# Kernel tuning notes

Hardware: AMD Instinct MI355X
Metric: run time of the kernel (lower is better)

## Reference

```python
import jax, jax.numpy as jnp
import numpy as np

CH = 256            # channels
IN_C = CH // 2      # 128
INTER_C = CH // 16  # 16
NUM_POINTS = 32
BN_EPS = 1e-5


def conv1x1(x, W, b=None):
    # x: [B,C,H,W], W: [O,C]
    y = jnp.einsum('oc,bchw->bohw', W, x)
    if b is not None:
        y = y + b[None, :, None, None]
    return y


def bilinear_sample(feat, sx, sy):
    """feat [B,C,H,W]; sx,sy [B,N,P] continuous index coords; border padding."""
    B, C, H, W = feat.shape
    x0f = jnp.floor(sx)
    y0f = jnp.floor(sy)
    wx = sx - x0f
    wy = sy - y0f
    x0 = jnp.clip(x0f.astype(jnp.int32), 0, W - 1)
    x1 = jnp.clip(x0f.astype(jnp.int32) + 1, 0, W - 1)
    y0 = jnp.clip(y0f.astype(jnp.int32), 0, H - 1)
    y1 = jnp.clip(y0f.astype(jnp.int32) + 1, 0, H - 1)
    feat_f = feat.reshape(B, C, H * W).transpose(0, 2, 1)  # [B,HW,C]

    def gather(yi, xi):
        idx = (yi * W + xi).reshape(B, -1)  # [B,N*P]
        return jnp.take_along_axis(feat_f, idx[:, :, None], axis=1)  # [B,N*P,C]

    wxf = wx.reshape(B, -1, 1)
    wyf = wy.reshape(B, -1, 1)
    out = (gather(y0, x0) * (1 - wxf) * (1 - wyf)
           + gather(y0, x1) * wxf * (1 - wyf)
           + gather(y1, x0) * (1 - wxf) * wyf
           + gather(y1, x1) * wxf * wyf)
    N, P = sx.shape[1], sx.shape[2]
    return out.reshape(B, N, P, C)


def multi_scale_attention(qf, vf, Wq, bq, Wk, bk, Wv, bv, Woff, boff):
    # deformable-style point-sampling attention with NUM_POINTS samples per query
    B, _, H, W = qf.shape
    N = H * W
    q = conv1x1(qf, Wq, bq).reshape(B, INTER_C, N).transpose(0, 2, 1)  # [B,N,Ci]
    k = conv1x1(vf, Wk, bk)                                            # [B,Ci,H,W]
    v = conv1x1(vf, Wv, bv)                                            # [B,Cv,H,W]
    off = conv1x1(qf, Woff, boff).reshape(B, NUM_POINTS, 2, N)
    off = off.transpose(0, 3, 1, 2)                                    # [B,N,P,2] (dx,dy)
    ys, xs = jnp.meshgrid(jnp.arange(H, dtype=qf.dtype),
                          jnp.arange(W, dtype=qf.dtype), indexing='ij')
    sx = xs.reshape(-1)[None, :, None] + off[..., 0]                   # [B,N,P]
    sy = ys.reshape(-1)[None, :, None] + off[..., 1]
    k_s = bilinear_sample(k, sx, sy)                                   # [B,N,P,Ci]
    v_s = bilinear_sample(v, sx, sy)                                   # [B,N,P,Cv]
    logits = jnp.einsum('bnc,bnpc->bnp', q, k_s) / jnp.sqrt(jnp.asarray(INTER_C, qf.dtype))
    attn = jax.nn.softmax(logits, axis=-1)
    out = jnp.einsum('bnp,bnpc->bnc', attn, v_s)                       # [B,N,Cv]
    return out.transpose(0, 2, 1).reshape(B, -1, H, W)


def setup_inputs() -> dict:
    key = jax.random.key(0)
    ks = jax.random.split(key, 12)
    B, Hl, Wl, Hh, Wh = 2, 64, 64, 32, 32
    s = 0.02
    return {
        'low_feature': jax.random.normal(ks[0], (B, CH, Hl, Wl), jnp.float32),
        'high_feature': jax.random.normal(ks[1], (B, CH, Hh, Wh), jnp.float32),
        'W1': jax.random.normal(ks[2], (IN_C, 2 * CH), jnp.float32) * s,
        'b1': jnp.zeros((IN_C,), jnp.float32),
        'W2': jax.random.normal(ks[3], (IN_C, CH), jnp.float32) * s,
        'b2': jnp.zeros((IN_C,), jnp.float32),
        'Wq': jax.random.normal(ks[4], (INTER_C, IN_C), jnp.float32) * s,
        'bq': jnp.zeros((INTER_C,), jnp.float32),
        'Wk': jax.random.normal(ks[5], (INTER_C, IN_C), jnp.float32) * s,
        'bk': jnp.zeros((INTER_C,), jnp.float32),
        'Wv': jax.random.normal(ks[6], (IN_C, IN_C), jnp.float32) * s,
        'bv': jnp.zeros((IN_C,), jnp.float32),
        'Woff': jax.random.normal(ks[7], (2 * NUM_POINTS, IN_C), jnp.float32) * 0.5,
        'boff': jnp.zeros((2 * NUM_POINTS,), jnp.float32),
        'Wb': jax.random.normal(ks[8], (CH, IN_C + CH), jnp.float32) * s,
        'gamma': jnp.ones((CH,), jnp.float32),
        'beta': jnp.zeros((CH,), jnp.float32),
        'rmean': jnp.zeros((CH,), jnp.float32),
        'rvar': jnp.ones((CH,), jnp.float32),
    }


def reference(low_feature, high_feature, W1, b1, W2, b2, Wq, bq, Wk, bk,
              Wv, bv, Woff, boff, Wb, gamma, beta, rmean, rvar):
    B, _, Hl, Wl = low_feature.shape
    # F.interpolate(mode='bilinear', align_corners=False) == jax.image half-pixel bilinear
    high_up = jax.image.resize(high_feature, (B, CH, Hl, Wl), method='bilinear')
    query_feature = conv1x1(jnp.concatenate([high_up, low_feature], axis=1), W1, b1)
    value_feature = conv1x1(high_up, W2, b2)
    value_feature = multi_scale_attention(query_feature, value_feature,
                                          Wq, bq, Wk, bk, Wv, bv, Woff, boff)
    x = conv1x1(jnp.concatenate([value_feature, high_up], axis=1), Wb)
    # BatchNorm (eval form) + ReLU
    x = (x - rmean[None, :, None, None]) * jax.lax.rsqrt(rvar + BN_EPS)[None, :, None, None]
    x = x * gamma[None, :, None, None] + beta[None, :, None, None]
    return jax.nn.relu(x)
```

## Files before the change

kernel.cpp:

```cpp
#include <hip/hip_runtime.h>
#include <hip/hip_bf16.h>

#define NL 4096
#define HH 32
#define WH 32

typedef __attribute__((ext_vector_type(8))) short s8v;
typedef __attribute__((ext_vector_type(4))) short s4v;
typedef __attribute__((ext_vector_type(4))) float f32x4;

static __device__ inline unsigned short f2bf(float x) {
  __hip_bfloat16 h = __float2bfloat16(x);
  return *reinterpret_cast<unsigned short*>(&h);
}
static __device__ inline float bfbits2f(unsigned int lo16) {
  unsigned int u = lo16 << 16;
  return *reinterpret_cast<float*>(&u);
}
static __device__ inline int swizzle_wg(int b) {
  return ((b & 7) << 6) | (b >> 3);
}

__global__ __launch_bounds__(256) void convert_weights_k(
    const float* __restrict__ w1, const float* __restrict__ w2,
    const float* __restrict__ wq, const float* __restrict__ woff,
    const float* __restrict__ wk, const float* __restrict__ wv,
    const float* __restrict__ wb, short* __restrict__ dst) {
  int i = (blockIdx.x * 256 + threadIdx.x) * 4;
  const float* src; int off;
  if      (i <  65536) { src = w1;   off = 0; }
  else if (i <  98304) { src = w2;   off = 65536; }
  else if (i < 100352) { src = wq;   off = 98304; }
  else if (i < 108544) { src = woff; off = 100352; }
  else if (i < 110592) { src = wk;   off = 108544; }
  else if (i < 126976) { src = wv;   off = 110592; }
  else if (i < 225280) { src = wb;   off = 126976; }
  else return;
  float4 v = *(const float4*)(src + (i - off));
  s4v o;
  o[0] = (short)f2bf(v.x); o[1] = (short)f2bf(v.y);
  o[2] = (short)f2bf(v.z); o[3] = (short)f2bf(v.w);
  *(s4v*)(dst + i) = o;
}

__global__ __launch_bounds__(512, 4) void k1_fused(
    const float* __restrict__ low, const float* __restrict__ high,
    const short* __restrict__ wc,
    const float* __restrict__ b1, const float* __restrict__ b2,
    const float* __restrict__ bq, const float* __restrict__ boff,
    const float* __restrict__ bk, const float* __restrict__ bv,
    short* __restrict__ xh, float* __restrict__ q_t, float* __restrict__ k_t,
    float* __restrict__ off_t, short* __restrict__ v_t) {
  __shared__ short xin_s[16 * 520];
  __shared__ short qf_s[16 * 136];
  __shared__ short vf_s[16 * 136];
  const int tid = threadIdx.x;
  const int wg = swizzle_wg(blockIdx.x);
  const int pix0 = wg * 16;
  const int b = pix0 >> 12;
  const int n0 = pix0 & (NL - 1);

  {
    const int nl = tid & 15, cg = tid >> 4;
    const int n = n0 + nl;
    const int y = n >> 6, x = n & 63;
    float sx = x * 0.5f - 0.25f;
    float sy = y * 0.5f - 0.25f;
    float x0f = floorf(sx), y0f = floorf(sy);
    float wx = sx - x0f, wy = sy - y0f;
    int x0i = (int)x0f, y0i = (int)y0f;
    int x0c = min(WH - 1, max(0, x0i)), x1c = min(WH - 1, max(0, x0i + 1));
    int y0c = min(HH - 1, max(0, y0i)), y1c = min(HH - 1, max(0, y0i + 1));
    float w00 = (1.f - wy) * (1.f - wx), w01 = (1.f - wy) * wx;
    float w10 = wy * (1.f - wx),         w11 = wy * wx;
#pragma unroll
    for (int i = 0; i < 8; i++) {
      int c = cg * 8 + i;
      const float* f = high + (size_t)(b * 256 + c) * (HH * WH);
      float v = w00 * f[y0c * WH + x0c] + w01 * f[y0c * WH + x1c]
              + w10 * f[y1c * WH + x0c] + w11 * f[y1c * WH + x1c];
      xin_s[nl * 520 + c] = (short)f2bf(v);
      xin_s[nl * 520 + 256 + c] =
          (short)f2bf(low[(size_t)(b * 256 + c) * NL + n]);
    }
  }
  __syncthreads();

  {
    const int r = tid >> 5, c0 = (tid & 31) * 8;
    s8v v0 = *(const s8v*)(xin_s + r * 520 + c0);
    *(s8v*)(xh + (size_t)(pix0 + r) * 256 + c0) = v0;
  }

  const int wave = tid >> 6, lane = tid & 63;
  const int quad = lane >> 4, id = lane & 15;

  {
    f32x4 acc = (f32x4){0.f, 0.f, 0.f, 0.f};
    const short* a0 = wc + (size_t)(wave * 16 + id) * 512 + quad * 8;
    const short* bp = xin_s + id * 520 + quad * 8;
#pragma unroll
    for (int kk = 0; kk < 512; kk += 32)
      acc = __builtin_amdgcn_mfma_f32_16x16x32_bf16(
          *(const s8v*)(a0 + kk), *(const s8v*)(bp + kk), acc, 0, 0, 0);
    int m0 = wave * 16 + quad * 4;
    s4v o0;
#pragma unroll
    for (int r = 0; r < 4; r++) o0[r] = (short)f2bf(acc[r] + b1[m0 + r]);
    *(s4v*)(qf_s + id * 136 + m0) = o0;
  }

  {
    f32x4 acc = (f32x4){0.f, 0.f, 0.f, 0.f};
    const short* a0 = wc + 65536 + (size_t)(wave * 16 + id) * 256 + quad * 8;
    const short* bp = xin_s + id * 520 + quad * 8;
#pragma unroll
    for (int kk = 0; kk < 256; kk += 32)
      acc = __builtin_amdgcn_mfma_f32_16x16x32_bf16(
          *(const s8v*)(a0 + kk), *(const s8v*)(bp + kk), acc, 0, 0, 0);
    int m0 = wave * 16 + quad * 4;
    s4v o0;
#pragma unroll
    for (int r = 0; r < 4; r++) o0[r] = (short)f2bf(acc[r] + b2[m0 + r]);
    *(s4v*)(vf_s + id * 136 + m0) = o0;
  }
  __syncthreads();

  for (int f = wave; f < 14; f += 8) {
    const short* ap = wc + 98304 + (size_t)(f * 16 + id) * 128 + quad * 8;
    const short* bp = (f < 5 ? qf_s : vf_s) + id * 136 + quad * 8;
    f32x4 acc = (f32x4){0.f, 0.f, 0.f, 0.f};
#pragma unroll
    for (int kk = 0; kk < 128; kk += 32)
      acc = __builtin_amdgcn_mfma_f32_16x16x32_bf16(
          *(const s8v*)(ap + kk), *(const s8v*)(bp + kk), acc, 0, 0, 0);
    const int pix = pix0 + id;
    const int mq = quad * 4;
    if (f == 0) {
      f32x4 v;
#pragma unroll
      for (int r = 0; r < 4; r++) v[r] = acc[r] + bq[mq + r];
      *(f32x4*)(q_t + (size_t)pix * 16 + mq) = v;
    } else if (f < 5) {
      int m = (f - 1) * 16 + mq;
      f32x4 v;
#pragma unroll
      for (int r = 0; r < 4; r++) v[r] = acc[r] + boff[m + r];
      *(f32x4*)(off_t + (size_t)pix * 64 + m) = v;
    } else if (f == 5) {
      f32x4 v;
#pragma unroll
      for (int r = 0; r < 4; r++) v[r] = acc[r] + bk[mq + r];
      *(f32x4*)(k_t + (size_t)pix * 16 + mq) = v;
    } else {
      int m = (f - 6) * 16 + mq;
      s4v o;
#pragma unroll
      for (int r = 0; r < 4; r++) o[r] = (short)f2bf(acc[r] + bv[m + r]);
      *(s4v*)(v_t + (size_t)pix * 128 + m) = o;
    }
  }
}

__global__ __launch_bounds__(1024, 2) void k2_fused(
    const float* __restrict__ q_t, const float* __restrict__ k_t,
    const short* __restrict__ v_t, const float* __restrict__ off_t,
    const short* __restrict__ xh, const short* __restrict__ wb,
    const float* __restrict__ gamma, const float* __restrict__ beta,
    const float* __restrict__ rmean, const float* __restrict__ rvar,
    float* __restrict__ out) {
  __shared__ float2 s_wi[16][32][4];
  __shared__ short attn_s[16 * 136];
  const int tid = threadIdx.x;
  const int wave = tid >> 6, lane = tid & 63;
  const int wg = swizzle_wg(blockIdx.x);
  const int pix0 = wg * 16;

  {
    const int qidx = pix0 + wave;
    const int b = qidx >> 12;
    const int n = qidx & (NL - 1);
    const int qy = n >> 6, qx = n & 63;

    const int pt = lane >> 1, h = lane & 1;
    float2 dxy = *(const float2*)(off_t + (size_t)qidx * 64 + 2 * pt);

    const float* qp = q_t + (size_t)qidx * 16;
    float qreg[16];
#pragma unroll
    for (int i = 0; i < 16; i += 4) {
      float4 t4 = *(const float4*)(qp + i);
      qreg[i] = t4.x; qreg[i + 1] = t4.y; qreg[i + 2] = t4.z; qreg[i + 3] = t4.w;
    }

    float sx = (float)qx + dxy.x;
    float sy = (float)qy + dxy.y;
    float x0f = floorf(sx), y0f = floorf(sy);
    float wx = sx - x0f, wy = sy - y0f;
    int x0i = (int)x0f, y0i = (int)y0f;
    int x0 = min(63, max(0, x0i)), x1 = min(63, max(0, x0i + 1));
    int y0 = min(63, max(0, y0i)), y1 = min(63, max(0, y0i + 1));

    int   yr  = h ? y1 : y0;
    float wyr = h ? wy : (1.f - wy);
    int   pa = yr * 64 + x0, pb = yr * 64 + x1;
    float wa = wyr * (1.f - wx), wb_ = wyr * wx;

    const float* kb = k_t + (size_t)b * NL * 16;
    float da = 0.f, db = 0.f;
    {
      const float* ka = kb + (size_t)pa * 16;
      const float* kc = kb + (size_t)pb * 16;
#pragma unroll
      for (int i = 0; i < 16; i += 4) {
        float4 a4 = *(const float4*)(ka + i);
        float4 c4 = *(const float4*)(kc + i);
        da = fmaf(qreg[i], a4.x, da); da = fmaf(qreg[i + 1], a4.y, da);
        da = fmaf(qreg[i + 2], a4.z, da); da = fmaf(qreg[i + 3], a4.w, da);
        db = fmaf(qreg[i], c4.x, db); db = fmaf(qreg[i + 1], c4.y, db);
        db = fmaf(qreg[i + 2], c4.z, db); db = fmaf(qreg[i + 3], c4.w, db);
      }
    }
    float part = wa * da + wb_ * db;
    part += __shfl_xor(part, 1, 64);
    float logit = part * 0.25f;

    float e = __expf(logit);

    s_wi[wave][pt][2 * h + 0] = make_float2(e * wa,  __int_as_float(pa << 7));
    s_wi[wave][pt][2 * h + 1] = make_float2(e * wb_, __int_as_float(pb << 7));

    const int t = lane >> 4, chunk = lane & 15;
    const short* vb = v_t + (size_t)b * NL * 128 + chunk * 8;
    float o[8];
#pragma unroll
    for (int j = 0; j < 8; j++) o[j] = 0.f;
    for (int base = 0; base < 32; base += 8) {
      float w8[8]; int ix[8];
#pragma unroll
      for (int j = 0; j < 8; j++) {
        float2 wi = s_wi[wave][base + j][t];
        w8[j] = wi.x;
        ix[j] = __float_as_int(wi.y);
      }
      uint4 u[8];
#pragma unroll
      for (int j = 0; j < 8; j++) u[j] = *(const uint4*)(vb + ix[j]);
#pragma unroll
      for (int j = 0; j < 8; j++) {
        o[0] = fmaf(w8[j], bfbits2f(u[j].x & 0xffffu), o[0]);
        o[1] = fmaf(w8[j], bfbits2f(u[j].x >> 16),     o[1]);
        o[2] = fmaf(w8[j], bfbits2f(u[j].y & 0xffffu), o[2]);
        o[3] = fmaf(w8[j], bfbits2f(u[j].y >> 16),     o[3]);
        o[4] = fmaf(w8[j], bfbits2f(u[j].z & 0xffffu), o[4]);
        o[5] = fmaf(w8[j], bfbits2f(u[j].z >> 16),     o[5]);
        o[6] = fmaf(w8[j], bfbits2f(u[j].w & 0xffffu), o[6]);
        o[7] = fmaf(w8[j], bfbits2f(u[j].w >> 16),     o[7]);
      }
    }
    float ssum = e;
#pragma unroll
    for (int s = 32; s > 0; s >>= 1) ssum += __shfl_xor(ssum, s, 64);
    float scale = 2.f / ssum;

#pragma unroll
    for (int j = 0; j < 8; j++) {
      o[j] += __shfl_xor(o[j], 16, 64);
      o[j] += __shfl_xor(o[j], 32, 64);
    }
    if (t == 0) {
      uint4 pk;
      pk.x = (unsigned)f2bf(o[0] * scale) | ((unsigned)f2bf(o[1] * scale) << 16);
      pk.y = (unsigned)f2bf(o[2] * scale) | ((unsigned)f2bf(o[3] * scale) << 16);
      pk.z = (unsigned)f2bf(o[4] * scale) | ((unsigned)f2bf(o[5] * scale) << 16);
      pk.w = (unsigned)f2bf(o[6] * scale) | ((unsigned)f2bf(o[7] * scale) << 16);
      *(uint4*)(attn_s + wave * 136 + chunk * 8) = pk;
    }
  }
  __syncthreads();

  {
    const int quad = lane >> 4, id = lane & 15;
    const int m0 = wave * 16;
    const int pix = pix0 + id;

    f32x4 acc = (f32x4){0.f, 0.f, 0.f, 0.f};
    const short* ap = wb + (size_t)(m0 + id) * 384 + quad * 8;
    const short* bs = attn_s + id * 136 + quad * 8;
    const short* bg = xh + (size_t)pix * 256 + quad * 8;
#pragma unroll
    for (int k = 0; k < 4; k++)
      acc = __builtin_amdgcn_mfma_f32_16x16x32_bf16(
          *(const s8v*)(ap + k * 32), *(const s8v*)(bs + k * 32), acc, 0, 0, 0);
#pragma unroll
    for (int k = 0; k < 8; k++)
      acc = __builtin_amdgcn_mfma_f32_16x16x32_bf16(
          *(const s8v*)(ap + 128 + k * 32), *(const s8v*)(bg + k * 32), acc, 0, 0, 0);

    const int bb = pix >> 12, nlow = pix & (NL - 1);
    const int mbase = m0 + quad * 4;
#pragma unroll
    for (int r = 0; r < 4; r++) {
      int o = mbase + r;
      float s  = gamma[o] * rsqrtf(rvar[o] + 1e-5f);
      float sh = beta[o] - rmean[o] * s;
      __builtin_nontemporal_store(fmaxf(fmaf(acc[r], s, sh), 0.f),
                                  &out[((size_t)bb * 256 + o) * NL + nlow]);
    }
  }
}

extern "C" void kernel_launch(void* const* d_in, const int* in_sizes, int n_in,
                              void* d_out, int out_size, void* d_ws, size_t ws_size,
                              hipStream_t stream) {
  const float* low   = (const float*)d_in[0];
  const float* high  = (const float*)d_in[1];
  const float* W1    = (const float*)d_in[2];
  const float* b1    = (const float*)d_in[3];
  const float* W2    = (const float*)d_in[4];
  const float* b2    = (const float*)d_in[5];
  const float* Wq    = (const float*)d_in[6];
  const float* bq    = (const float*)d_in[7];
  const float* Wk    = (const float*)d_in[8];
  const float* bk    = (const float*)d_in[9];
  const float* Wv    = (const float*)d_in[10];
  const float* bv    = (const float*)d_in[11];
  const float* Woff  = (const float*)d_in[12];
  const float* boff  = (const float*)d_in[13];
  const float* Wb    = (const float*)d_in[14];
  const float* gamma = (const float*)d_in[15];
  const float* beta  = (const float*)d_in[16];
  const float* rmean = (const float*)d_in[17];
  const float* rvar  = (const float*)d_in[18];
  float* out = (float*)d_out;

  short* ws    = (short*)d_ws;
  short* xh    = ws;
  short* v_t   = xh + 2097152;
  short* wc    = v_t + 1048576;
  float* q_t   = (float*)(wc + 225280);
  float* k_t   = q_t + 131072;
  float* off_t = k_t + 131072;

  convert_weights_k<<<220, 256, 0, stream>>>(W1, W2, Wq, Woff, Wk, Wv, Wb, wc);
  k1_fused<<<512, 512, 0, stream>>>(low, high, wc, b1, b2, bq, boff, bk, bv,
                                    xh, q_t, k_t, off_t, v_t);
  k2_fused<<<512, 1024, 0, stream>>>(q_t, k_t, v_t, off_t, xh, wc + 126976,
                                     gamma, beta, rmean, rvar, out);
}
```

Baseline: 151.5 us.

## Move upsample and input packing into weight-conversion prep kernel

The bilinear upsampling of high_feature and the bf16 packing of low_feature move out of k1 into the weight-conversion kernel. That kernel now launches 512 blocks and writes a packed [pix,512] bf16 buffer to global memory, which k1 then just loads into shared memory. k2 reads the upsampled half of that buffer instead of a separate xh copy. The aim is to take the gather-heavy prep off k1's critical path and spread it across more work per launch. The cost is an extra round trip of 8 MB through global memory and a larger workspace.

```diff
diff --git a/kernel.cpp b/kernel.cpp
--- a/kernel.cpp
+++ b/kernel.cpp
@@ -21,35 +21,73 @@
   return ((b & 7) << 6) | (b >> 3);
 }
 
-__global__ __launch_bounds__(256) void convert_weights_k(
+__global__ __launch_bounds__(256) void prep_k(
+    const float* __restrict__ low, const float* __restrict__ high,
     const float* __restrict__ w1, const float* __restrict__ w2,
     const float* __restrict__ wq, const float* __restrict__ woff,
     const float* __restrict__ wk, const float* __restrict__ wv,
-    const float* __restrict__ wb, short* __restrict__ dst) {
-  int i = (blockIdx.x * 256 + threadIdx.x) * 4;
-  const float* src; int off;
-  if      (i <  65536) { src = w1;   off = 0; }
-  else if (i <  98304) { src = w2;   off = 65536; }
-  else if (i < 100352) { src = wq;   off = 98304; }
-  else if (i < 108544) { src = woff; off = 100352; }
-  else if (i < 110592) { src = wk;   off = 108544; }
-  else if (i < 126976) { src = wv;   off = 110592; }
-  else if (i < 225280) { src = wb;   off = 126976; }
-  else return;
-  float4 v = *(const float4*)(src + (i - off));
-  s4v o;
-  o[0] = (short)f2bf(v.x); o[1] = (short)f2bf(v.y);
-  o[2] = (short)f2bf(v.z); o[3] = (short)f2bf(v.w);
-  *(s4v*)(dst + i) = o;
-}
-
-__global__ __launch_bounds__(512, 4) void k1_fused(
-    const float* __restrict__ low, const float* __restrict__ high,
-    const short* __restrict__ wc,
+    const float* __restrict__ wb, short* __restrict__ wc,
+    short* __restrict__ xin_g) {
+  const int tid = threadIdx.x, bidx = blockIdx.x;
+
+  if (bidx < 220) {
+    int i = (bidx * 256 + tid) * 4;
+    if (i < 225280) {
+      const float* src; int off;
+      if      (i <  65536) { src = w1;   off = 0; }
+      else if (i <  98304) { src = w2;   off = 65536; }
+      else if (i < 100352) { src = wq;   off = 98304; }
+      else if (i < 108544) { src = woff; off = 100352; }
+      else if (i < 110592) { src = wk;   off = 108544; }
+      else if (i < 126976) { src = wv;   off = 110592; }
+      else                 { src = wb;   off = 126976; }
+      float4 v = *(const float4*)(src + (i - off));
+      s4v o;
+      o[0] = (short)f2bf(v.x); o[1] = (short)f2bf(v.y);
+      o[2] = (short)f2bf(v.z); o[3] = (short)f2bf(v.w);
+      *(s4v*)(wc + i) = o;
+    }
+  }
+
+  const int pix0 = bidx * 16;
+  const int b = pix0 >> 12;
+  const int n0 = pix0 & (NL - 1);
+  const int nl = tid & 15, cg = tid >> 4;
+  const int n = n0 + nl;
+  const int y = n >> 6, x = n & 63;
+  float sx = x * 0.5f - 0.25f;
+  float sy = y * 0.5f - 0.25f;
+  float x0f = floorf(sx), y0f = floorf(sy);
+  float wx = sx - x0f, wy = sy - y0f;
+  int x0i = (int)x0f, y0i = (int)y0f;
+  int x0c = min(WH - 1, max(0, x0i)), x1c = min(WH - 1, max(0, x0i + 1));
+  int y0c = min(HH - 1, max(0, y0i)), y1c = min(HH - 1, max(0, y0i + 1));
+  float w00 = (1.f - wy) * (1.f - wx), w01 = (1.f - wy) * wx;
+  float w10 = wy * (1.f - wx),         w11 = wy * wx;
+
+  short hi[16], lo[16];
+#pragma unroll
+  for (int i = 0; i < 16; i++) {
+    int c = cg * 16 + i;
+    const float* f = high + (size_t)(b * 256 + c) * (HH * WH);
+    float v = w00 * f[y0c * WH + x0c] + w01 * f[y0c * WH + x1c]
+            + w10 * f[y1c * WH + x0c] + w11 * f[y1c * WH + x1c];
+    hi[i] = (short)f2bf(v);
+    lo[i] = (short)f2bf(low[(size_t)(b * 256 + c) * NL + n]);
+  }
+  short* dst = xin_g + (size_t)(pix0 + nl) * 512 + cg * 16;
+  *(s8v*)(dst)       = *(const s8v*)(hi);
+  *(s8v*)(dst + 8)   = *(const s8v*)(hi + 8);
+  *(s8v*)(dst + 256) = *(const s8v*)(lo);
+  *(s8v*)(dst + 264) = *(const s8v*)(lo + 8);
+}
+
+__global__ __launch_bounds__(512, 4) void k1_gemm(
+    const short* __restrict__ xin_g, const short* __restrict__ wc,
     const float* __restrict__ b1, const float* __restrict__ b2,
     const float* __restrict__ bq, const float* __restrict__ boff,
     const float* __restrict__ bk, const float* __restrict__ bv,
-    short* __restrict__ xh, float* __restrict__ q_t, float* __restrict__ k_t,
+    float* __restrict__ q_t, float* __restrict__ k_t,
     float* __restrict__ off_t, short* __restrict__ v_t) {
   __shared__ short xin_s[16 * 520];
   __shared__ short qf_s[16 * 136];
@@ -57,40 +95,16 @@
   const int tid = threadIdx.x;
   const int wg = swizzle_wg(blockIdx.x);
   const int pix0 = wg * 16;
-  const int b = pix0 >> 12;
-  const int n0 = pix0 & (NL - 1);
-
-  {
-    const int nl = tid & 15, cg = tid >> 4;
-    const int n = n0 + nl;
-    const int y = n >> 6, x = n & 63;
-    float sx = x * 0.5f - 0.25f;
-    float sy = y * 0.5f - 0.25f;
-    float x0f = floorf(sx), y0f = floorf(sy);
-    float wx = sx - x0f, wy = sy - y0f;
-    int x0i = (int)x0f, y0i = (int)y0f;
-    int x0c = min(WH - 1, max(0, x0i)), x1c = min(WH - 1, max(0, x0i + 1));
-    int y0c = min(HH - 1, max(0, y0i)), y1c = min(HH - 1, max(0, y0i + 1));
-    float w00 = (1.f - wy) * (1.f - wx), w01 = (1.f - wy) * wx;
-    float w10 = wy * (1.f - wx),         w11 = wy * wx;
-#pragma unroll
-    for (int i = 0; i < 8; i++) {
-      int c = cg * 8 + i;
-      const float* f = high + (size_t)(b * 256 + c) * (HH * WH);
-      float v = w00 * f[y0c * WH + x0c] + w01 * f[y0c * WH + x1c]
-              + w10 * f[y1c * WH + x0c] + w11 * f[y1c * WH + x1c];
-      xin_s[nl * 520 + c] = (short)f2bf(v);
-      xin_s[nl * 520 + 256 + c] =
-          (short)f2bf(low[(size_t)(b * 256 + c) * NL + n]);
-    }
+
+  {
+    const int r = tid >> 5, c0 = (tid & 31) * 16;
+    const short* src = xin_g + (size_t)(pix0 + r) * 512 + c0;
+    s8v v0 = *(const s8v*)(src);
+    s8v v1 = *(const s8v*)(src + 8);
+    *(s8v*)(xin_s + r * 520 + c0) = v0;
+    *(s8v*)(xin_s + r * 520 + c0 + 8) = v1;
   }
   __syncthreads();
-
-  {
-    const int r = tid >> 5, c0 = (tid & 31) * 8;
-    s8v v0 = *(const s8v*)(xin_s + r * 520 + c0);
-    *(s8v*)(xh + (size_t)(pix0 + r) * 256 + c0) = v0;
-  }
 
   const int wave = tid >> 6, lane = tid & 63;
   const int quad = lane >> 4, id = lane & 15;
@@ -165,7 +179,7 @@
 __global__ __launch_bounds__(1024, 2) void k2_fused(
     const float* __restrict__ q_t, const float* __restrict__ k_t,
     const short* __restrict__ v_t, const float* __restrict__ off_t,
-    const short* __restrict__ xh, const short* __restrict__ wb,
+    const short* __restrict__ xin_g, const short* __restrict__ wb,
     const float* __restrict__ gamma, const float* __restrict__ beta,
     const float* __restrict__ rmean, const float* __restrict__ rvar,
     float* __restrict__ out) {
@@ -287,7 +301,7 @@
     f32x4 acc = (f32x4){0.f, 0.f, 0.f, 0.f};
     const short* ap = wb + (size_t)(m0 + id) * 384 + quad * 8;
     const short* bs = attn_s + id * 136 + quad * 8;
-    const short* bg = xh + (size_t)pix * 256 + quad * 8;
+    const short* bg = xin_g + (size_t)pix * 512 + quad * 8;
 #pragma unroll
     for (int k = 0; k < 4; k++)
       acc = __builtin_amdgcn_mfma_f32_16x16x32_bf16(
@@ -335,16 +349,17 @@
   float* out = (float*)d_out;
 
   short* ws    = (short*)d_ws;
-  short* xh    = ws;
-  short* v_t   = xh + 2097152;
+  short* xin_g = ws;
+  short* v_t   = xin_g + 4194304;
   short* wc    = v_t + 1048576;
   float* q_t   = (float*)(wc + 225280);
   float* k_t   = q_t + 131072;
   float* off_t = k_t + 131072;
 
-  convert_weights_k<<<220, 256, 0, stream>>>(W1, W2, Wq, Woff, Wk, Wv, Wb, wc);
-  k1_fused<<<512, 512, 0, stream>>>(low, high, wc, b1, b2, bq, boff, bk, bv,
-                                    xh, q_t, k_t, off_t, v_t);
-  k2_fused<<<512, 1024, 0, stream>>>(q_t, k_t, v_t, off_t, xh, wc + 126976,
+  prep_k<<<512, 256, 0, stream>>>(low, high, W1, W2, Wq, Woff, Wk, Wv, Wb,
+                                  wc, xin_g);
+  k1_gemm<<<512, 512, 0, stream>>>(xin_g, wc, b1, b2, bq, boff, bk, bv,
+                                   q_t, k_t, off_t, v_t);
+  k2_fused<<<512, 1024, 0, stream>>>(q_t, k_t, v_t, off_t, xin_g, wc + 126976,
                                      gamma, beta, rmean, rvar, out);
 }
```

Measured after the change: 156.6 us. 1.03x slower.
